# Performance work log

Measured on AMD Instinct MI355X. Metric: run time of the kernel, lower is better.

Reference implementation:

```python
import jax, jax.numpy as jnp
import numpy as np

TAU_MEM = 20.0
TAU_SYN = 5.0
ALPHA_MEM = float(np.exp(-1.0 / TAU_MEM))
ALPHA_SYN = float(np.exp(-1.0 / TAU_SYN))
CONNECTIVITY = 0.1
SPECTRAL_RADIUS = 0.9


def setup_inputs() -> dict:
    key = jax.random.key(0)
    k1, k2, k3, k4 = jax.random.split(key, 4)
    B, D, N = 2048, 256, 512
    rates = jax.random.normal(k1, (B, D), dtype=jnp.float32)
    input_weight = jax.random.normal(k2, (N, D), dtype=jnp.float32) * 0.1
    W = jax.random.normal(k3, (N, N), dtype=jnp.float32)
    mask = (jax.random.uniform(k4, (N, N)) < CONNECTIVITY).astype(jnp.float32)
    W = W * mask
    # mirror torch init: scale by spectral_radius / max eigvalsh
    max_eig = jnp.linalg.eigvalsh(W)[-1]
    W = W * (SPECTRAL_RADIUS / max_eig)
    return {
        "rates": rates,
        "input_weight": input_weight,
        "reservoir_weight": W,
        "v_mem": jnp.zeros((B, N), dtype=jnp.float32),
        "current": jnp.zeros((B, N), dtype=jnp.float32),
        "n_steps": 64,
    }


def reference(rates, input_weight, reservoir_weight, v_mem, current, n_steps):
    dtype = rates.dtype
    # input current is identical every step in the original loop -> hoist it
    input_current = rates @ input_weight.T  # (B, N)

    def step(carry, _):
        v, c, spike_sum = carry
        rec = (c > 0).astype(dtype) @ reservoir_weight  # (B, N)
        c = ALPHA_SYN * c + (1.0 - ALPHA_SYN) * (input_current + rec)
        v = ALPHA_MEM * v + (1.0 - ALPHA_MEM) * c
        spike_sum = spike_sum + (v > 0).astype(dtype)
        return (v, c, spike_sum), None

    (v, c, spike_sum), _ = jax.lax.scan(
        step, (v_mem, current, jnp.zeros_like(v_mem)), None, length=n_steps
    )
    readout = spike_sum / n_steps  # == stack(spikes).mean(dim=1)
    return readout, (v, c)
```

## Files before the change

### kernel.cpp

```cpp
#include <hip/hip_runtime.h>
#include <stdint.h>


#define N_NEU 512
#define B_ROWS 2048
#define D_IN 256
#define R_PB 8
#define NBLK (B_ROWS / R_PB)

#define WS_PERM    0
#define WS_RANK    2048
#define WS_CNT     4096
#define WS_CNTW    8192
#define WS_IBASE   8256
#define WS_WBASE   8320
#define WS_IDX     16384
#define WS_WT      81920

#define SPK_OFF(k)  ((k) << 4)
#define SPK_BUF     8192

#define H16_ONE 0x3C00u

__global__ __launch_bounds__(256) void lsm_count(
    const float* __restrict__ W, uint32_t* __restrict__ ws)
{
    int t  = threadIdx.x;
    int k0 = blockIdx.x * 4;
    int c0 = 0, c1 = 0;
    #pragma unroll
    for (int kk = 0; kk < 4; ++kk) {
        const float* row = W + (size_t)(k0 + kk) * N_NEU;
        c0 += (row[t]       != 0.0f) ? 1 : 0;
        c1 += (row[t + 256] != 0.0f) ? 1 : 0;
    }
    if (c0) atomicAdd(&ws[(WS_CNT >> 2) + t],       (uint32_t)c0);
    if (c1) atomicAdd(&ws[(WS_CNT >> 2) + t + 256], (uint32_t)c1);
}

__global__ __launch_bounds__(512) void lsm_sort(uint32_t* __restrict__ ws)
{
    __shared__ int hist[N_NEU + 1];
    __shared__ int csort[N_NEU];
    __shared__ int gcw[8];

    int t = threadIdx.x;
    int creal = (int)ws[(WS_CNT >> 2) + t];
    for (int i = t; i < N_NEU + 1; i += 512) hist[i] = 0;
    __syncthreads();
    atomicAdd(&hist[creal], 1);
    __syncthreads();
    if (t == 0) {
        int acc = 0;
        for (int v = 0; v <= N_NEU; ++v) { int h = hist[v]; hist[v] = acc; acc += h; }
    }
    __syncthreads();
    int rank = atomicAdd(&hist[creal], 1);
    ws[(WS_PERM >> 2) + rank] = (uint32_t)t;
    ws[(WS_RANK >> 2) + t]    = (uint32_t)rank;
    csort[rank] = creal;
    __syncthreads();
    if (t < 8) {
        int cw = csort[t * 64 + 63];
        cw = (cw + 7) & ~7;
        gcw[t] = cw;
        ws[(WS_CNTW >> 2) + t] = (uint32_t)cw;
    }
    __syncthreads();
    if (t == 0) {
        int ai = 0, aw = 0;
        for (int g = 0; g < 8; ++g) {
            ws[(WS_IBASE >> 2) + g] = (uint32_t)ai;
            ws[(WS_WBASE >> 2) + g] = (uint32_t)aw;
            ai += gcw[g] * 64 * 2;
            aw += gcw[g] * 64 * 4;
        }
    }
    __syncthreads();
    int wg = rank >> 6, ls = rank & 63;
    int cw = gcw[wg];
    uint32_t ib = ws[(WS_IBASE >> 2) + wg];
    uint32_t wb = ws[(WS_WBASE >> 2) + wg];
    char* base = (char*)ws;
    for (int j = creal; j < cw; ++j) {
        *(unsigned short*)(base + WS_IDX + ib + (j >> 3) * 1024 + ls * 16 + (j & 7) * 2) = 0;
        *(float*)(base + WS_WT + wb + (j >> 3) * 2048 + ls * 32 + (j & 7) * 4) = 0.0f;
    }
}

__global__ __launch_bounds__(64) void lsm_fill(
    const float* __restrict__ W, uint32_t* __restrict__ ws)
{
    int c    = blockIdx.x;
    int lane = threadIdx.x;
    char* base = (char*)ws;
    uint32_t rank = ws[(WS_RANK >> 2) + c];
    int wg = (int)(rank >> 6), ls = (int)(rank & 63);
    uint32_t ib = ws[(WS_IBASE >> 2) + wg];
    uint32_t wb = ws[(WS_WBASE >> 2) + wg];
    int rot = ls & 7;

    __shared__ int bcnt[8];
    __shared__ int bcur[8];
    if (lane < 8) bcnt[lane] = 0;
    __syncthreads();

    for (int k = lane; k < N_NEU; k += 64) {
        float wv = W[(size_t)k * N_NEU + c];
        if (wv != 0.0f) {
            int r = ((k & 7) - rot) & 7;
            atomicAdd(&bcnt[r], 1);
        }
    }
    __syncthreads();
    if (lane == 0) {
        int acc = 0;
        for (int r = 0; r < 8; ++r) { bcur[r] = acc; acc += bcnt[r]; }
    }
    __syncthreads();

    for (int k = lane; k < N_NEU; k += 64) {
        float wv = W[(size_t)k * N_NEU + c];
        if (wv != 0.0f) {
            int r = ((k & 7) - rot) & 7;
            int j = atomicAdd(&bcur[r], 1);
            *(unsigned short*)(base + WS_IDX + ib + (j >> 3) * 1024 + ls * 16 + (j & 7) * 2)
                = (unsigned short)SPK_OFF(k);
            *(float*)(base + WS_WT + wb + (j >> 3) * 2048 + ls * 32 + (j & 7) * 4) = wv;
        }
    }
}

#define GATH(P, X, B) \
    P##0 = *(const uint4*)((B) + ((X).x & 0xffffu)); \
    P##1 = *(const uint4*)((B) + ((X).x >> 16));     \
    P##2 = *(const uint4*)((B) + ((X).y & 0xffffu)); \
    P##3 = *(const uint4*)((B) + ((X).y >> 16));     \
    P##4 = *(const uint4*)((B) + ((X).z & 0xffffu)); \
    P##5 = *(const uint4*)((B) + ((X).z >> 16));     \
    P##6 = *(const uint4*)((B) + ((X).w & 0xffffu)); \
    P##7 = *(const uint4*)((B) + ((X).w >> 16));

#define FMIX_LO(ACC, WV, S) \
    asm("v_fma_mix_f32 %0, %1, %2, %0 op_sel:[0,0,0] op_sel_hi:[0,1,0]" \
        : "+v"(ACC) : "v"(WV), "v"(S));
#define FMIX_HI(ACC, WV, S) \
    asm("v_fma_mix_f32 %0, %1, %2, %0 op_sel:[0,1,0] op_sel_hi:[0,1,0]" \
        : "+v"(ACC) : "v"(WV), "v"(S));

#define C1(S, WV) \
    FMIX_LO(rec0, WV, (S).x) FMIX_HI(rec1, WV, (S).x) \
    FMIX_LO(rec2, WV, (S).y) FMIX_HI(rec3, WV, (S).y) \
    FMIX_LO(rec4, WV, (S).z) FMIX_HI(rec5, WV, (S).z) \
    FMIX_LO(rec6, WV, (S).w) FMIX_HI(rec7, WV, (S).w)

#define CONS(P, WA, WB) \
    C1(P##0, (WA).x) C1(P##1, (WA).y) C1(P##2, (WA).z) C1(P##3, (WA).w) \
    C1(P##4, (WB).x) C1(P##5, (WB).y) C1(P##6, (WB).z) C1(P##7, (WB).w)

#define LDW(WA, WB, K) \
    WA = ((const float4*)(wp0 + (K) * 2048))[0]; \
    WB = ((const float4*)(wp0 + (K) * 2048))[1];

__global__ __launch_bounds__(512, 1)
void lsm_main(
    const float* __restrict__ rates, const float* __restrict__ inW,
    const float* __restrict__ vin,   const float* __restrict__ cin,
    const int* __restrict__ nsteps_p,
    const uint32_t* __restrict__ ws, float* __restrict__ out)
{
    __shared__ __align__(16) unsigned char smem[2 * SPK_BUF + 16384];
    float* stg = (float*)(smem + 2 * SPK_BUF);
    float* rl  = stg;

    int q    = threadIdx.x;
    int blk  = blockIdx.x;
    int r0   = blk * R_PB;
    int w    = q >> 6;
    int lane = q & 63;
    int wg   = (w < 4) ? w : (11 - w);
    int n    = (int)ws[(WS_PERM >> 2) + wg * 64 + lane];
    int cw   = (int)ws[(WS_CNTW >> 2) + wg];
    int nit  = cw >> 3;
    const char* ip0 = (const char*)ws + WS_IDX + ws[(WS_IBASE >> 2) + wg]
                    + lane * 16;
    const char* wp0 = (const char*)ws + WS_WT  + ws[(WS_WBASE >> 2) + wg]
                    + lane * 32;
    int spk_n = SPK_OFF(n);

    float c0v[R_PB], v0v[R_PB];
    #pragma unroll
    for (int r = 0; r < R_PB; ++r)
        stg[r * N_NEU + q] = cin[(size_t)(r0 + r) * N_NEU + q];
    __syncthreads();
    #pragma unroll
    for (int r = 0; r < R_PB; ++r) c0v[r] = stg[r * N_NEU + n];
    __syncthreads();
    #pragma unroll
    for (int r = 0; r < R_PB; ++r)
        stg[r * N_NEU + q] = vin[(size_t)(r0 + r) * N_NEU + q];
    __syncthreads();
    #pragma unroll
    for (int r = 0; r < R_PB; ++r) v0v[r] = stg[r * N_NEU + n];
    __syncthreads();

    ((float4*)rl)[q] = ((const float4*)(rates + (size_t)r0 * D_IN))[q];
    __syncthreads();

    float I[R_PB] = {0.f, 0.f, 0.f, 0.f, 0.f, 0.f, 0.f, 0.f};
    {
        const float4* wrow = (const float4*)(inW + (size_t)n * D_IN);
        for (int d4 = 0; d4 < D_IN / 4; ++d4) {
            float4 wv = wrow[d4];
            #pragma unroll
            for (int r = 0; r < R_PB; ++r) {
                const float* rr = rl + r * D_IN + d4 * 4;
                I[r] += wv.x * rr[0] + wv.y * rr[1] + wv.z * rr[2] + wv.w * rr[3];
            }
        }
    }

    uint4 sini = make_uint4(0u, 0u, 0u, 0u);
    #pragma unroll
    for (int r = 0; r < R_PB; ++r) {
        unsigned hb = (c0v[r] > 0.f) ? H16_ONE : 0u;
        unsigned sh = (r & 1) ? 16 : 0;
        if (r < 2)      sini.x |= hb << sh;
        else if (r < 4) sini.y |= hb << sh;
        else if (r < 6) sini.z |= hb << sh;
        else            sini.w |= hb << sh;
    }
    *(uint4*)(smem + spk_n) = sini;

    unsigned ssx = 0u, ssy = 0u;

    uint4 xr0, xr1, xr2, xr3, xr4, xr5, xr6, xr7, xr8, xr9, xr10, xr11;
    const uint4 xz = make_uint4(0u, 0u, 0u, 0u);
    xr0  =              *(const uint4*)(ip0);
    xr1  = (1  < nit) ? *(const uint4*)(ip0 + 1024)  : xz;
    xr2  = (2  < nit) ? *(const uint4*)(ip0 + 2048)  : xz;
    xr3  = (3  < nit) ? *(const uint4*)(ip0 + 3072)  : xz;
    xr4  = (4  < nit) ? *(const uint4*)(ip0 + 4096)  : xz;
    xr5  = (5  < nit) ? *(const uint4*)(ip0 + 5120)  : xz;
    xr6  = (6  < nit) ? *(const uint4*)(ip0 + 6144)  : xz;
    xr7  = (7  < nit) ? *(const uint4*)(ip0 + 7168)  : xz;
    xr8  = (8  < nit) ? *(const uint4*)(ip0 + 8192)  : xz;
    xr9  = (9  < nit) ? *(const uint4*)(ip0 + 9216)  : xz;
    xr10 = (10 < nit) ? *(const uint4*)(ip0 + 10240) : xz;
    xr11 = (11 < nit) ? *(const uint4*)(ip0 + 11264) : xz;

    const float AS   = (float)0.8187307530779818;
    const float OMAS = (float)(1.0 - 0.8187307530779818);
    const float AM   = (float)0.9512294245007140;
    const float OMAM = (float)(1.0 - 0.9512294245007140);

    int T = nsteps_p[0];
    __syncthreads();

    #pragma unroll 1
    for (int t = 0; t < T; ++t) {
        const unsigned char* sb = smem + ((t & 1) ? SPK_BUF : 0);
        unsigned char*       db = smem + ((t & 1) ? 0 : SPK_BUF);

        float rec0 = 0.f, rec1 = 0.f, rec2 = 0.f, rec3 = 0.f;
        float rec4 = 0.f, rec5 = 0.f, rec6 = 0.f, rec7 = 0.f;
        uint4 a0, a1, a2, a3, a4, a5, a6, a7;
        uint4 b0, b1, b2, b3, b4, b5, b6, b7;
        float4 waA, wbA, waB, wbB;

        LDW(waA, wbA, 0)
        GATH(a, xr0, sb)
        if (1 < nit)  { LDW(waB, wbB, 1)  GATH(b, xr1, sb)  }
        CONS(a, waA, wbA)
        if (1 < nit)  {
            if (2 < nit)  { LDW(waA, wbA, 2)  GATH(a, xr2, sb)  }
            CONS(b, waB, wbB)
        }
        if (2 < nit)  {
            if (3 < nit)  { LDW(waB, wbB, 3)  GATH(b, xr3, sb)  }
            CONS(a, waA, wbA)
        }
        if (3 < nit)  {
            if (4 < nit)  { LDW(waA, wbA, 4)  GATH(a, xr4, sb)  }
            CONS(b, waB, wbB)
        }
        if (4 < nit)  {
            if (5 < nit)  { LDW(waB, wbB, 5)  GATH(b, xr5, sb)  }
            CONS(a, waA, wbA)
        }
        if (5 < nit)  {
            if (6 < nit)  { LDW(waA, wbA, 6)  GATH(a, xr6, sb)  }
            CONS(b, waB, wbB)
        }
        if (6 < nit)  {
            if (7 < nit)  { LDW(waB, wbB, 7)  GATH(b, xr7, sb)  }
            CONS(a, waA, wbA)
        }
        if (7 < nit)  {
            if (8 < nit)  { LDW(waA, wbA, 8)  GATH(a, xr8, sb)  }
            CONS(b, waB, wbB)
        }
        if (8 < nit)  {
            if (9 < nit)  { LDW(waB, wbB, 9)  GATH(b, xr9, sb)  }
            CONS(a, waA, wbA)
        }
        if (9 < nit)  {
            if (10 < nit) { LDW(waA, wbA, 10) GATH(a, xr10, sb) }
            CONS(b, waB, wbB)
        }
        if (10 < nit) {
            if (11 < nit) { LDW(waB, wbB, 11) GATH(b, xr11, sb) }
            CONS(a, waA, wbA)
        }
        if (11 < nit) {
            CONS(b, waB, wbB)
        }

        uint4 ns = make_uint4(0u, 0u, 0u, 0u);
        unsigned vbx = 0u, vby = 0u;
        {
            float rca[R_PB] = {rec0, rec1, rec2, rec3, rec4, rec5, rec6, rec7};
            #pragma unroll
            for (int r = 0; r < R_PB; ++r) {
                c0v[r] = AS * c0v[r] + OMAS * (I[r] + rca[r]);
                v0v[r] = AM * v0v[r] + OMAM * c0v[r];
                unsigned hb = (c0v[r] > 0.f) ? H16_ONE : 0u;
                unsigned vb = (v0v[r] > 0.f) ? 1u : 0u;
                unsigned sh = (r & 1) ? 16 : 0;
                if (r < 2)      ns.x |= hb << sh;
                else if (r < 4) ns.y |= hb << sh;
                else if (r < 6) ns.z |= hb << sh;
                else            ns.w |= hb << sh;
                if (r < 4) vbx |= vb << (r * 8);
                else       vby |= vb << ((r - 4) * 8);
            }
        }
        ssx += vbx;
        ssy += vby;
        *(uint4*)(db + spk_n) = ns;
        __syncthreads();
    }

    float invT = 1.0f / (float)T;
    size_t BN = (size_t)B_ROWS * N_NEU;

    #pragma unroll
    for (int r = 0; r < R_PB; ++r) {
        unsigned cnt = (r < 4) ? ((ssx >> (r * 8)) & 0xffu)
                               : ((ssy >> ((r - 4) * 8)) & 0xffu);
        stg[r * N_NEU + n] = (float)cnt * invT;
    }
    __syncthreads();
    #pragma unroll
    for (int r = 0; r < R_PB; ++r)
        out[(size_t)(r0 + r) * N_NEU + q] = stg[r * N_NEU + q];
    __syncthreads();

    #pragma unroll
    for (int r = 0; r < R_PB; ++r) stg[r * N_NEU + n] = v0v[r];
    __syncthreads();
    #pragma unroll
    for (int r = 0; r < R_PB; ++r)
        out[BN + (size_t)(r0 + r) * N_NEU + q] = stg[r * N_NEU + q];
    __syncthreads();

    #pragma unroll
    for (int r = 0; r < R_PB; ++r) stg[r * N_NEU + n] = c0v[r];
    __syncthreads();
    #pragma unroll
    for (int r = 0; r < R_PB; ++r)
        out[2 * BN + (size_t)(r0 + r) * N_NEU + q] = stg[r * N_NEU + q];
}

extern "C" void kernel_launch(void* const* d_in, const int* in_sizes, int n_in,
                              void* d_out, int out_size, void* d_ws, size_t ws_size,
                              hipStream_t stream)
{
    const float* rates = (const float*)d_in[0];
    const float* inW   = (const float*)d_in[1];
    const float* W     = (const float*)d_in[2];
    const float* vin   = (const float*)d_in[3];
    const float* cin   = (const float*)d_in[4];
    const int*   nst   = (const int*)d_in[5];
    uint32_t* ws = (uint32_t*)d_ws;
    float* out = (float*)d_out;
    (void)in_sizes; (void)n_in; (void)out_size; (void)ws_size;

    hipMemsetAsync((char*)d_ws + WS_CNT, 0, 2048, stream);

    lsm_count<<<128, 256, 0, stream>>>(W, ws);
    lsm_sort<<<1, 512, 0, stream>>>(ws);
    lsm_fill<<<N_NEU, 64, 0, stream>>>(W, ws);
    lsm_main<<<NBLK, 512, 0, stream>>>(rates, inW, vin, cin, nst, ws, out);
}
```

Before: 326.1 us.

## Split sparse recurrent gather across two half-blocks and rebalance fill by bank

Doubles the main kernel's block size to 1024 threads so that two wave halves each process half of a neuron's nonzero list, then combines the partial sums through shared memory before the state update. This aims to cut per-thread serial latency in the sparse spike gather. It costs an extra barrier and a shared-memory exchange per step, and the second half sits idle during the update. The fill kernel is rewritten with ballot-based compaction and bank-balanced slot assignment, and padding slots are now filled there with zero weights instead of in the sort kernel.

```diff
diff --git a/kernel.cpp b/kernel.cpp
--- a/kernel.cpp
+++ b/kernel.cpp
@@ -21,6 +21,7 @@
 #define SPK_BUF     8192
 
 #define H16_ONE 0x3C00u
+#define MAXPB   32
 
 __global__ __launch_bounds__(256) void lsm_count(
     const float* __restrict__ W, uint32_t* __restrict__ ws)
@@ -76,16 +77,6 @@
             aw += gcw[g] * 64 * 4;
         }
     }
-    __syncthreads();
-    int wg = rank >> 6, ls = rank & 63;
-    int cw = gcw[wg];
-    uint32_t ib = ws[(WS_IBASE >> 2) + wg];
-    uint32_t wb = ws[(WS_WBASE >> 2) + wg];
-    char* base = (char*)ws;
-    for (int j = creal; j < cw; ++j) {
-        *(unsigned short*)(base + WS_IDX + ib + (j >> 3) * 1024 + ls * 16 + (j & 7) * 2) = 0;
-        *(float*)(base + WS_WT + wb + (j >> 3) * 2048 + ls * 32 + (j & 7) * 4) = 0.0f;
-    }
 }
 
 __global__ __launch_bounds__(64) void lsm_fill(
@@ -94,40 +85,63 @@
     int c    = blockIdx.x;
     int lane = threadIdx.x;
     char* base = (char*)ws;
+
     uint32_t rank = ws[(WS_RANK >> 2) + c];
-    int wg = (int)(rank >> 6), ls = (int)(rank & 63);
-    uint32_t ib = ws[(WS_IBASE >> 2) + wg];
-    uint32_t wb = ws[(WS_WBASE >> 2) + wg];
-    int rot = ls & 7;
-
-    __shared__ int bcnt[8];
-    __shared__ int bcur[8];
-    if (lane < 8) bcnt[lane] = 0;
-    __syncthreads();
-
-    for (int k = lane; k < N_NEU; k += 64) {
+    int ls = (int)(rank & 63), g = (int)(rank >> 6);
+    int cw = (int)ws[(WS_CNTW >> 2) + g];
+    uint32_t ib = ws[(WS_IBASE >> 2) + g];
+    uint32_t wb = ws[(WS_WBASE >> 2) + g];
+
+    __shared__ unsigned short ent_k[8][MAXPB];
+    __shared__ float          ent_w[8][MAXPB];
+    __shared__ int            nb[8];
+
+    int bm = lane & 7;
+    unsigned long long mbk   = 0x0101010101010101ULL << bm;
+    unsigned long long below = (1ULL << lane) - 1;
+    int myBase = 0;
+    for (int i = 0; i < 8; ++i) {
+        int k = lane + 64 * i;
         float wv = W[(size_t)k * N_NEU + c];
-        if (wv != 0.0f) {
-            int r = ((k & 7) - rot) & 7;
-            atomicAdd(&bcnt[r], 1);
-        }
-    }
-    __syncthreads();
-    if (lane == 0) {
-        int acc = 0;
-        for (int r = 0; r < 8; ++r) { bcur[r] = acc; acc += bcnt[r]; }
-    }
-    __syncthreads();
-
-    for (int k = lane; k < N_NEU; k += 64) {
-        float wv = W[(size_t)k * N_NEU + c];
-        if (wv != 0.0f) {
-            int r = ((k & 7) - rot) & 7;
-            int j = atomicAdd(&bcur[r], 1);
-            *(unsigned short*)(base + WS_IDX + ib + (j >> 3) * 1024 + ls * 16 + (j & 7) * 2)
-                = (unsigned short)SPK_OFF(k);
-            *(float*)(base + WS_WT + wb + (j >> 3) * 2048 + ls * 32 + (j & 7) * 4) = wv;
-        }
+        bool nz = (wv != 0.0f);
+        unsigned long long bal = __ballot(nz);
+        if (nz) {
+            int p = myBase + __popcll(bal & mbk & below);
+            ent_k[bm][p] = (unsigned short)k;
+            ent_w[bm][p] = wv;
+        }
+        myBase += __popcll(bal & mbk);
+    }
+    if (lane < 8) nb[lane] = myBase;
+    __syncthreads();
+
+    int Q = cw >> 3;
+    for (int j = lane; j < cw; j += 64) {
+        int b = (j + ls) & 7;
+        int m = j >> 3;
+        int nbb = nb[b];
+        int d = (nbb < Q) ? nbb : Q;
+        unsigned short kk; float wv;
+        if (m < d) {
+            kk = ent_k[b][m]; wv = ent_w[b][m];
+        } else {
+            int f = m - d;
+            for (int bp = 0; bp < b; ++bp) {
+                int nn = nb[bp];
+                f += (Q > nn) ? (Q - nn) : 0;
+            }
+            int acc = 0, bsel = -1, isel = 0;
+            for (int bp = 0; bp < 8; ++bp) {
+                int ov = nb[bp] - Q; ov = (ov > 0) ? ov : 0;
+                if (bsel < 0 && f < acc + ov) { bsel = bp; isel = Q + (f - acc); }
+                acc += ov;
+            }
+            if (bsel >= 0) { kk = ent_k[bsel][isel]; wv = ent_w[bsel][isel]; }
+            else           { kk = (unsigned short)b; wv = 0.0f; }
+        }
+        *(unsigned short*)(base + WS_IDX + ib + (j >> 3) * 1024 + ls * 16 + (j & 7) * 2)
+            = (unsigned short)SPK_OFF(kk);
+        *(float*)(base + WS_WT + wb + (j >> 3) * 2048 + ls * 32 + (j & 7) * 4) = wv;
     }
 }
 
@@ -162,53 +176,62 @@
     WA = ((const float4*)(wp0 + (K) * 2048))[0]; \
     WB = ((const float4*)(wp0 + (K) * 2048))[1];
 
-__global__ __launch_bounds__(512, 1)
+__global__ __launch_bounds__(1024)
 void lsm_main(
     const float* __restrict__ rates, const float* __restrict__ inW,
     const float* __restrict__ vin,   const float* __restrict__ cin,
     const int* __restrict__ nsteps_p,
     const uint32_t* __restrict__ ws, float* __restrict__ out)
 {
-    __shared__ __align__(16) unsigned char smem[2 * SPK_BUF + 16384];
-    float* stg = (float*)(smem + 2 * SPK_BUF);
-    float* rl  = stg;
+    __shared__ __align__(16) unsigned char smem[2 * SPK_BUF + 16384 + 16384];
+    float* stg  = (float*)(smem + 2 * SPK_BUF);
+    float* rl   = stg;
+    float* pbuf = (float*)(smem + 2 * SPK_BUF + 16384);
 
     int q    = threadIdx.x;
     int blk  = blockIdx.x;
     int r0   = blk * R_PB;
     int w    = q >> 6;
     int lane = q & 63;
-    int wg   = (w < 4) ? w : (11 - w);
+    int half = w >> 3;
+    int wp   = w & 7;
+    int wg   = (wp < 4) ? wp : (11 - wp);
     int n    = (int)ws[(WS_PERM >> 2) + wg * 64 + lane];
     int cw   = (int)ws[(WS_CNTW >> 2) + wg];
     int nit  = cw >> 3;
+    int nh   = (nit + 1) >> 1;
+    int nw   = half ? (nit - nh) : nh;
     const char* ip0 = (const char*)ws + WS_IDX + ws[(WS_IBASE >> 2) + wg]
-                    + lane * 16;
+                    + lane * 16 + (half ? nh * 1024 : 0);
     const char* wp0 = (const char*)ws + WS_WT  + ws[(WS_WBASE >> 2) + wg]
-                    + lane * 32;
+                    + lane * 32 + (half ? nh * 2048 : 0);
     int spk_n = SPK_OFF(n);
+    float* pb = pbuf + wg * 512 + lane;
 
     float c0v[R_PB], v0v[R_PB];
-    #pragma unroll
-    for (int r = 0; r < R_PB; ++r)
-        stg[r * N_NEU + q] = cin[(size_t)(r0 + r) * N_NEU + q];
-    __syncthreads();
-    #pragma unroll
-    for (int r = 0; r < R_PB; ++r) c0v[r] = stg[r * N_NEU + n];
-    __syncthreads();
-    #pragma unroll
-    for (int r = 0; r < R_PB; ++r)
-        stg[r * N_NEU + q] = vin[(size_t)(r0 + r) * N_NEU + q];
-    __syncthreads();
-    #pragma unroll
-    for (int r = 0; r < R_PB; ++r) v0v[r] = stg[r * N_NEU + n];
-    __syncthreads();
-
-    ((float4*)rl)[q] = ((const float4*)(rates + (size_t)r0 * D_IN))[q];
+    for (int i = q; i < R_PB * N_NEU; i += 1024)
+        stg[i] = cin[(size_t)r0 * N_NEU + i];
+    __syncthreads();
+    if (!half) {
+        #pragma unroll
+        for (int r = 0; r < R_PB; ++r) c0v[r] = stg[r * N_NEU + n];
+    }
+    __syncthreads();
+    for (int i = q; i < R_PB * N_NEU; i += 1024)
+        stg[i] = vin[(size_t)r0 * N_NEU + i];
+    __syncthreads();
+    if (!half) {
+        #pragma unroll
+        for (int r = 0; r < R_PB; ++r) v0v[r] = stg[r * N_NEU + n];
+    }
+    __syncthreads();
+
+    if (q < (R_PB * D_IN) / 4)
+        ((float4*)rl)[q] = ((const float4*)(rates + (size_t)r0 * D_IN))[q];
     __syncthreads();
 
     float I[R_PB] = {0.f, 0.f, 0.f, 0.f, 0.f, 0.f, 0.f, 0.f};
-    {
+    if (!half) {
         const float4* wrow = (const float4*)(inW + (size_t)n * D_IN);
         for (int d4 = 0; d4 < D_IN / 4; ++d4) {
             float4 wv = wrow[d4];
@@ -218,36 +241,29 @@
                 I[r] += wv.x * rr[0] + wv.y * rr[1] + wv.z * rr[2] + wv.w * rr[3];
             }
         }
-    }
-
-    uint4 sini = make_uint4(0u, 0u, 0u, 0u);
-    #pragma unroll
-    for (int r = 0; r < R_PB; ++r) {
-        unsigned hb = (c0v[r] > 0.f) ? H16_ONE : 0u;
-        unsigned sh = (r & 1) ? 16 : 0;
-        if (r < 2)      sini.x |= hb << sh;
-        else if (r < 4) sini.y |= hb << sh;
-        else if (r < 6) sini.z |= hb << sh;
-        else            sini.w |= hb << sh;
-    }
-    *(uint4*)(smem + spk_n) = sini;
+        uint4 sini = make_uint4(0u, 0u, 0u, 0u);
+        #pragma unroll
+        for (int r = 0; r < R_PB; ++r) {
+            unsigned hb = (c0v[r] > 0.f) ? H16_ONE : 0u;
+            unsigned sh = (r & 1) ? 16 : 0;
+            if (r < 2)      sini.x |= hb << sh;
+            else if (r < 4) sini.y |= hb << sh;
+            else if (r < 6) sini.z |= hb << sh;
+            else            sini.w |= hb << sh;
+        }
+        *(uint4*)(smem + spk_n) = sini;
+    }
 
     unsigned ssx = 0u, ssy = 0u;
 
-    uint4 xr0, xr1, xr2, xr3, xr4, xr5, xr6, xr7, xr8, xr9, xr10, xr11;
+    uint4 xr0, xr1, xr2, xr3, xr4, xr5;
     const uint4 xz = make_uint4(0u, 0u, 0u, 0u);
-    xr0  =              *(const uint4*)(ip0);
-    xr1  = (1  < nit) ? *(const uint4*)(ip0 + 1024)  : xz;
-    xr2  = (2  < nit) ? *(const uint4*)(ip0 + 2048)  : xz;
-    xr3  = (3  < nit) ? *(const uint4*)(ip0 + 3072)  : xz;
-    xr4  = (4  < nit) ? *(const uint4*)(ip0 + 4096)  : xz;
-    xr5  = (5  < nit) ? *(const uint4*)(ip0 + 5120)  : xz;
-    xr6  = (6  < nit) ? *(const uint4*)(ip0 + 6144)  : xz;
-    xr7  = (7  < nit) ? *(const uint4*)(ip0 + 7168)  : xz;
-    xr8  = (8  < nit) ? *(const uint4*)(ip0 + 8192)  : xz;
-    xr9  = (9  < nit) ? *(const uint4*)(ip0 + 9216)  : xz;
-    xr10 = (10 < nit) ? *(const uint4*)(ip0 + 10240) : xz;
-    xr11 = (11 < nit) ? *(const uint4*)(ip0 + 11264) : xz;
+    xr0 = (0 < nw) ? *(const uint4*)(ip0)        : xz;
+    xr1 = (1 < nw) ? *(const uint4*)(ip0 + 1024) : xz;
+    xr2 = (2 < nw) ? *(const uint4*)(ip0 + 2048) : xz;
+    xr3 = (3 < nw) ? *(const uint4*)(ip0 + 3072) : xz;
+    xr4 = (4 < nw) ? *(const uint4*)(ip0 + 4096) : xz;
+    xr5 = (5 < nw) ? *(const uint4*)(ip0 + 5120) : xz;
 
     const float AS   = (float)0.8187307530779818;
     const float OMAS = (float)(1.0 - 0.8187307530779818);
@@ -268,108 +284,95 @@
         uint4 b0, b1, b2, b3, b4, b5, b6, b7;
         float4 waA, wbA, waB, wbB;
 
-        LDW(waA, wbA, 0)
-        GATH(a, xr0, sb)
-        if (1 < nit)  { LDW(waB, wbB, 1)  GATH(b, xr1, sb)  }
-        CONS(a, waA, wbA)
-        if (1 < nit)  {
-            if (2 < nit)  { LDW(waA, wbA, 2)  GATH(a, xr2, sb)  }
+        if (0 < nw) { LDW(waA, wbA, 0)  GATH(a, xr0, sb) }
+        if (1 < nw) { LDW(waB, wbB, 1)  GATH(b, xr1, sb) }
+        if (0 < nw) { CONS(a, waA, wbA) }
+        if (1 < nw) {
+            if (2 < nw) { LDW(waA, wbA, 2)  GATH(a, xr2, sb) }
             CONS(b, waB, wbB)
         }
-        if (2 < nit)  {
-            if (3 < nit)  { LDW(waB, wbB, 3)  GATH(b, xr3, sb)  }
+        if (2 < nw) {
+            if (3 < nw) { LDW(waB, wbB, 3)  GATH(b, xr3, sb) }
             CONS(a, waA, wbA)
         }
-        if (3 < nit)  {
-            if (4 < nit)  { LDW(waA, wbA, 4)  GATH(a, xr4, sb)  }
+        if (3 < nw) {
+            if (4 < nw) { LDW(waA, wbA, 4)  GATH(a, xr4, sb) }
             CONS(b, waB, wbB)
         }
-        if (4 < nit)  {
-            if (5 < nit)  { LDW(waB, wbB, 5)  GATH(b, xr5, sb)  }
+        if (4 < nw) {
+            if (5 < nw) { LDW(waB, wbB, 5)  GATH(b, xr5, sb) }
             CONS(a, waA, wbA)
         }
-        if (5 < nit)  {
-            if (6 < nit)  { LDW(waA, wbA, 6)  GATH(a, xr6, sb)  }
-            CONS(b, waB, wbB)
-        }
-        if (6 < nit)  {
-            if (7 < nit)  { LDW(waB, wbB, 7)  GATH(b, xr7, sb)  }
-            CONS(a, waA, wbA)
-        }
-        if (7 < nit)  {
-            if (8 < nit)  { LDW(waA, wbA, 8)  GATH(a, xr8, sb)  }
-            CONS(b, waB, wbB)
-        }
-        if (8 < nit)  {
-            if (9 < nit)  { LDW(waB, wbB, 9)  GATH(b, xr9, sb)  }
-            CONS(a, waA, wbA)
-        }
-        if (9 < nit)  {
-            if (10 < nit) { LDW(waA, wbA, 10) GATH(a, xr10, sb) }
-            CONS(b, waB, wbB)
-        }
-        if (10 < nit) {
-            if (11 < nit) { LDW(waB, wbB, 11) GATH(b, xr11, sb) }
-            CONS(a, waA, wbA)
-        }
-        if (11 < nit) {
-            CONS(b, waB, wbB)
-        }
-
-        uint4 ns = make_uint4(0u, 0u, 0u, 0u);
-        unsigned vbx = 0u, vby = 0u;
-        {
-            float rca[R_PB] = {rec0, rec1, rec2, rec3, rec4, rec5, rec6, rec7};
-            #pragma unroll
-            for (int r = 0; r < R_PB; ++r) {
-                c0v[r] = AS * c0v[r] + OMAS * (I[r] + rca[r]);
-                v0v[r] = AM * v0v[r] + OMAM * c0v[r];
-                unsigned hb = (c0v[r] > 0.f) ? H16_ONE : 0u;
-                unsigned vb = (v0v[r] > 0.f) ? 1u : 0u;
-                unsigned sh = (r & 1) ? 16 : 0;
-                if (r < 2)      ns.x |= hb << sh;
-                else if (r < 4) ns.y |= hb << sh;
-                else if (r < 6) ns.z |= hb << sh;
-                else            ns.w |= hb << sh;
-                if (r < 4) vbx |= vb << (r * 8);
-                else       vby |= vb << ((r - 4) * 8);
+        if (5 < nw) { CONS(b, waB, wbB) }
+
+        if (half) {
+            pb[0]   = rec0; pb[64]  = rec1; pb[128] = rec2; pb[192] = rec3;
+            pb[256] = rec4; pb[320] = rec5; pb[384] = rec6; pb[448] = rec7;
+        }
+        __syncthreads();
+
+        if (!half) {
+            rec0 += pb[0];   rec1 += pb[64];  rec2 += pb[128]; rec3 += pb[192];
+            rec4 += pb[256]; rec5 += pb[320]; rec6 += pb[384]; rec7 += pb[448];
+
+            uint4 ns = make_uint4(0u, 0u, 0u, 0u);
+            unsigned vbx = 0u, vby = 0u;
+            {
+                float rca[R_PB] = {rec0, rec1, rec2, rec3, rec4, rec5, rec6, rec7};
+                #pragma unroll
+                for (int r = 0; r < R_PB; ++r) {
+                    c0v[r] = AS * c0v[r] + OMAS * (I[r] + rca[r]);
+                    v0v[r] = AM * v0v[r] + OMAM * c0v[r];
+                    unsigned hb = (c0v[r] > 0.f) ? H16_ONE : 0u;
+                    unsigned vb = (v0v[r] > 0.f) ? 1u : 0u;
+                    unsigned sh = (r & 1) ? 16 : 0;
+                    if (r < 2)      ns.x |= hb << sh;
+                    else if (r < 4) ns.y |= hb << sh;
+                    else if (r < 6) ns.z |= hb << sh;
+                    else            ns.w |= hb << sh;
+                    if (r < 4) vbx |= vb << (r * 8);
+                    else       vby |= vb << ((r - 4) * 8);
+                }
             }
-        }
-        ssx += vbx;
-        ssy += vby;
-        *(uint4*)(db + spk_n) = ns;
+            ssx += vbx;
+            ssy += vby;
+            *(uint4*)(db + spk_n) = ns;
+        }
         __syncthreads();
     }
 
     float invT = 1.0f / (float)T;
     size_t BN = (size_t)B_ROWS * N_NEU;
 
-    #pragma unroll
-    for (int r = 0; r < R_PB; ++r) {
-        unsigned cnt = (r < 4) ? ((ssx >> (r * 8)) & 0xffu)
-                               : ((ssy >> ((r - 4) * 8)) & 0xffu);
-        stg[r * N_NEU + n] = (float)cnt * invT;
-    }
-    __syncthreads();
-    #pragma unroll
-    for (int r = 0; r < R_PB; ++r)
-        out[(size_t)(r0 + r) * N_NEU + q] = stg[r * N_NEU + q];
-    __syncthreads();
-
-    #pragma unroll
-    for (int r = 0; r < R_PB; ++r) stg[r * N_NEU + n] = v0v[r];
-    __syncthreads();
-    #pragma unroll
-    for (int r = 0; r < R_PB; ++r)
-        out[BN + (size_t)(r0 + r) * N_NEU + q] = stg[r * N_NEU + q];
-    __syncthreads();
-
-    #pragma unroll
-    for (int r = 0; r < R_PB; ++r) stg[r * N_NEU + n] = c0v[r];
-    __syncthreads();
-    #pragma unroll
-    for (int r = 0; r < R_PB; ++r)
-        out[2 * BN + (size_t)(r0 + r) * N_NEU + q] = stg[r * N_NEU + q];
+    if (!half) {
+        #pragma unroll
+        for (int r = 0; r < R_PB; ++r) {
+            unsigned cnt = (r < 4) ? ((ssx >> (r * 8)) & 0xffu)
+                                   : ((ssy >> ((r - 4) * 8)) & 0xffu);
+            stg[r * N_NEU + n] = (float)cnt * invT;
+        }
+    }
+    __syncthreads();
+    for (int i = q; i < R_PB * N_NEU; i += 1024)
+        out[(size_t)r0 * N_NEU + i] = stg[i];
+    __syncthreads();
+
+    if (!half) {
+        #pragma unroll
+        for (int r = 0; r < R_PB; ++r) stg[r * N_NEU + n] = v0v[r];
+    }
+    __syncthreads();
+    for (int i = q; i < R_PB * N_NEU; i += 1024)
+        out[BN + (size_t)r0 * N_NEU + i] = stg[i];
+    __syncthreads();
+
+    if (!half) {
+        #pragma unroll
+        for (int r = 0; r < R_PB; ++r) stg[r * N_NEU + n] = c0v[r];
+    }
+    __syncthreads();
+    for (int i = q; i < R_PB * N_NEU; i += 1024)
+        out[2 * BN + (size_t)r0 * N_NEU + i] = stg[i];
 }
 
 extern "C" void kernel_launch(void* const* d_in, const int* in_sizes, int n_in,
@@ -391,5 +394,5 @@
     lsm_count<<<128, 256, 0, stream>>>(W, ws);
     lsm_sort<<<1, 512, 0, stream>>>(ws);
     lsm_fill<<<N_NEU, 64, 0, stream>>>(W, ws);
-    lsm_main<<<NBLK, 512, 0, stream>>>(rates, inW, vin, cin, nst, ws, out);
-}
+    lsm_main<<<NBLK, 1024, 0, stream>>>(rates, inW, vin, cin, nst, ws, out);
+}
```

New measurement: 410.5 us. +25.9%, slower.
